# Kernel tuning notes

Measured on AMD Instinct MI355X. Metric: run time of the kernel, lower is better.

The kernel has to match this reference:

```python
import jax, jax.numpy as jnp
import numpy as np

EPS = 1e-5

def _bn_relu(z, gamma, beta):
    # BatchNorm1d (training mode: biased batch stats) + ReLU, per-feature over batch dim
    mean = jnp.mean(z, axis=0)
    var = jnp.var(z, axis=0)  # biased, matches torch BN normalization
    zn = (z - mean) * jax.lax.rsqrt(var + EPS) * gamma + beta
    return jax.nn.relu(zn)


def setup_inputs() -> dict:
    key = jax.random.key(0)
    ks = jax.random.split(key, 16)
    N, D_IN, H, D_OUT = 2097152, 16, 32, 1
    def lin(kw, kb, fan_in, fan_out):
        bound = 1.0 / np.sqrt(fan_in)
        W = jax.random.uniform(kw, (fan_out, fan_in), jnp.float32, -bound, bound)
        b = jax.random.uniform(kb, (fan_out,), jnp.float32, -bound, bound)
        return W, b
    W1, b1 = lin(ks[0], ks[1], D_IN, H)
    W2, b2 = lin(ks[2], ks[3], H, H)
    W3, b3 = lin(ks[4], ks[5], H, H)
    W4, b4 = lin(ks[6], ks[7], H, D_OUT)
    x = jax.random.normal(ks[8], (N, D_IN), jnp.float32)
    return {
        "x": x,
        "W1": W1, "b1": b1, "g1": jnp.ones((H,), jnp.float32), "be1": jnp.zeros((H,), jnp.float32),
        "W2": W2, "b2": b2, "g2": jnp.ones((H,), jnp.float32), "be2": jnp.zeros((H,), jnp.float32),
        "W3": W3, "b3": b3, "g3": jnp.ones((H,), jnp.float32), "be3": jnp.zeros((H,), jnp.float32),
        "W4": W4, "b4": b4,
    }


def reference(x, W1, b1, g1, be1, W2, b2, g2, be2, W3, b3, g3, be3, W4, b4):
    p1 = _bn_relu(x @ W1.T + b1, g1, be1)    # [N, H]
    p2 = _bn_relu(p1 @ W2.T + b2, g2, be2)   # [N, H]
    p3 = _bn_relu(p2 @ W3.T + b3, g3, be3)   # [N, H]
    return p3 @ W4.T + b4                    # [N, 1]
```

## Files before the change

### kernel.cpp

```cpp
#include <hip/hip_runtime.h>

#define EPS 1e-5f
#define NTHR 256
#define NBLK 2048
#define NSLOT 16

typedef __bf16 bf16x8 __attribute__((ext_vector_type(8)));
typedef float f32x16 __attribute__((ext_vector_type(16)));


template<int DEPTH>
__global__ __launch_bounds__(NTHR) void k_fwd(
    const float* __restrict__ x, __bf16* __restrict__ xb,
    const float* __restrict__ W1, const float* __restrict__ b1,
    const float* __restrict__ g1, const float* __restrict__ be1,
    const float* __restrict__ W2, const float* __restrict__ b2,
    const float* __restrict__ g2, const float* __restrict__ be2,
    const float* __restrict__ W3, const float* __restrict__ b3,
    const float* __restrict__ g3, const float* __restrict__ be3,
    const float* __restrict__ W4, const float* __restrict__ b4,
    float* __restrict__ stats, float* __restrict__ out, int N)
{
    constexpr bool STATS = (DEPTH < 4);
    __shared__ float s_stat[3][64];
    __shared__ float s_a[3][32];
    __shared__ float s_e[3][32];
    __shared__ float s_w[NTHR / 64][64];

    const int tid = threadIdx.x;
    const float invN = 1.0f / (float)N;

    if (tid < 64) {
        #pragma unroll
        for (int L = 0; L < DEPTH - 1; ++L) {
            float a = 0.f;
            #pragma unroll
            for (int s = 0; s < NSLOT; ++s) a += stats[L * (NSLOT * 64) + s * 64 + tid];
            s_stat[L][tid] = a;
        }
    }
    __syncthreads();
    if (tid < 32) {
        const float* gs[3]  = {g1, g2, g3};
        const float* bes[3] = {be1, be2, be3};
        const float* bs[3]  = {b1, b2, b3};
        #pragma unroll
        for (int L = 0; L < DEPTH - 1; ++L) {
            float mu = s_stat[L][tid] * invN;
            float v  = s_stat[L][32 + tid] * invN - mu * mu;
            float a  = gs[L][tid] * rsqrtf(v + EPS);
            s_a[L][tid] = a;
            s_e[L][tid] = bs[L][tid] - mu + bes[L][tid] / a;
        }
    }
    __syncthreads();

    const int lane = tid & 63;
    const int h = lane >> 5;
    const int ml = lane & 31;

    bf16x8 w1f;
    {
        const float* p = W1 + ml * 16 + h * 8;
        #pragma unroll
        for (int j = 0; j < 8; ++j) w1f[j] = (__bf16)p[j];
    }
    bf16x8 w2f0 = {}, w2f1 = {}, w3f0 = {}, w3f1 = {};
    if (DEPTH >= 2) {
        #pragma unroll
        for (int kh = 0; kh < 2; ++kh)
            #pragma unroll
            for (int j = 0; j < 8; ++j) {
                int pk = (j & 3) + 8 * (j >> 2) + 4 * h + 16 * kh;
                float v = W2[ml * 32 + pk] * s_a[0][pk];
                if (kh == 0) w2f0[j] = (__bf16)v; else w2f1[j] = (__bf16)v;
            }
    }
    if (DEPTH >= 3) {
        #pragma unroll
        for (int kh = 0; kh < 2; ++kh)
            #pragma unroll
            for (int j = 0; j < 8; ++j) {
                int pk = (j & 3) + 8 * (j >> 2) + 4 * h + 16 * kh;
                float v = W3[ml * 32 + pk] * s_a[1][pk];
                if (kh == 0) w3f0[j] = (__bf16)v; else w3f1[j] = (__bf16)v;
            }
    }

    f32x16 c1, c2 = {}, c3 = {};
    float w4c[16];
    #pragma unroll
    for (int i = 0; i < 16; ++i) {
        int p = (i & 3) + 8 * (i >> 2) + 4 * h;
        c1[i] = (DEPTH == 1) ? b1[p] : s_e[0][p];
        if (DEPTH >= 2) c2[i] = (DEPTH == 2) ? b2[p] : s_e[1][p];
        if (DEPTH >= 3) c3[i] = (DEPTH == 3) ? b3[p] : s_e[2][p];
        if (DEPTH == 4) w4c[i] = W4[p] * s_a[2][p]; else w4c[i] = 0.f;
    }
    const float b4v = (DEPTH == 4) ? b4[0] : 0.f;

    const int ntiles = N >> 5;
    const int nwaves = NBLK * (NTHR / 64);
    const int gwave  = blockIdx.x * (NTHR / 64) + (tid >> 6);
    const int tpw    = ntiles / nwaves;
    const int rem    = ntiles - tpw * nwaves;
    const int t0     = gwave * tpw + (gwave < rem ? gwave : rem);
    const int cnt    = tpw + (gwave < rem ? 1 : 0);

    float sums[16], sqs[16];
    #pragma unroll
    for (int i = 0; i < 16; ++i) { sums[i] = 0.f; sqs[i] = 0.f; }

    auto tile = [&](int t, bf16x8 xf) {
        f32x16 a1 = __builtin_amdgcn_mfma_f32_32x32x16_bf16(w1f, xf, c1, 0, 0, 0);
        if (DEPTH == 1) {
            #pragma unroll
            for (int i = 0; i < 16; ++i) { sums[i] += a1[i]; sqs[i] = fmaf(a1[i], a1[i], sqs[i]); }
            return;
        }
        bf16x8 qa, qb;
        #pragma unroll
        for (int j = 0; j < 8; ++j) {
            qa[j] = (__bf16)fmaxf(a1[j], 0.f);
            qb[j] = (__bf16)fmaxf(a1[8 + j], 0.f);
        }
        f32x16 a2 = __builtin_amdgcn_mfma_f32_32x32x16_bf16(w2f0, qa, c2, 0, 0, 0);
        a2 = __builtin_amdgcn_mfma_f32_32x32x16_bf16(w2f1, qb, a2, 0, 0, 0);
        if (DEPTH == 2) {
            #pragma unroll
            for (int i = 0; i < 16; ++i) { sums[i] += a2[i]; sqs[i] = fmaf(a2[i], a2[i], sqs[i]); }
            return;
        }
        bf16x8 pa, pb;
        #pragma unroll
        for (int j = 0; j < 8; ++j) {
            pa[j] = (__bf16)fmaxf(a2[j], 0.f);
            pb[j] = (__bf16)fmaxf(a2[8 + j], 0.f);
        }
        f32x16 a3 = __builtin_amdgcn_mfma_f32_32x32x16_bf16(w3f0, pa, c3, 0, 0, 0);
        a3 = __builtin_amdgcn_mfma_f32_32x32x16_bf16(w3f1, pb, a3, 0, 0, 0);
        if (DEPTH == 3) {
            #pragma unroll
            for (int i = 0; i < 16; ++i) { sums[i] += a3[i]; sqs[i] = fmaf(a3[i], a3[i], sqs[i]); }
            return;
        }
        float o = 0.f;
        #pragma unroll
        for (int i = 0; i < 16; ++i) o = fmaf(w4c[i], fmaxf(a3[i], 0.f), o);
        o += __shfl_xor(o, 32);
        if (h == 0) out[(t << 5) + ml] = o + b4v;
    };

    auto cvt = [&](float4 a, float4 b) -> bf16x8 {
        bf16x8 xf;
        xf[0] = (__bf16)a.x; xf[1] = (__bf16)a.y; xf[2] = (__bf16)a.z; xf[3] = (__bf16)a.w;
        xf[4] = (__bf16)b.x; xf[5] = (__bf16)b.y; xf[6] = (__bf16)b.z; xf[7] = (__bf16)b.w;
        return xf;
    };

    if (DEPTH == 1) {
        const int nb4 = cnt & ~3;
        float4 ua[4], ub[4];
        auto load4 = [&](int i0, float4* a, float4* b) {
            #pragma unroll
            for (int k = 0; k < 4; ++k) {
                const float4* p = (const float4*)(x + (size_t)((((t0 + i0 + k)) << 5) + ml) * 16 + h * 8);
                a[k] = p[0]; b[k] = p[1];
            }
        };
        auto comp4 = [&](int i0, const float4* a, const float4* b) {
            bf16x8 xf[4];
            #pragma unroll
            for (int k = 0; k < 4; ++k) xf[k] = cvt(a[k], b[k]);
            __bf16* w = xb + ((size_t)(t0 + i0) * 64 + lane) * 8;
            #pragma unroll
            for (int k = 0; k < 4; ++k) *(bf16x8*)(w + k * 512) = xf[k];
            #pragma unroll
            for (int k = 0; k < 4; ++k) tile(t0 + i0 + k, xf[k]);
        };
        int i0 = 0;
        if (nb4) load4(0, ua, ub);
        for (; i0 + 4 < nb4; i0 += 4) {
            float4 va[4], vb[4];
            load4(i0 + 4, va, vb);
            comp4(i0, ua, ub);
            #pragma unroll
            for (int k = 0; k < 4; ++k) { ua[k] = va[k]; ub[k] = vb[k]; }
        }
        if (nb4) { comp4(i0, ua, ub); i0 = nb4; }
        for (; i0 < cnt; ++i0) {
            const float4* p = (const float4*)(x + (size_t)(((t0 + i0) << 5) + ml) * 16 + h * 8);
            bf16x8 xf = cvt(p[0], p[1]);
            *(bf16x8*)(xb + ((size_t)(t0 + i0) * 64 + lane) * 8) = xf;
            tile(t0 + i0, xf);
        }
    } else {
        const int nb8 = cnt & ~7;
        int i0 = 0;
        for (; i0 < nb8; i0 += 8) {
            const __bf16* r = xb + ((size_t)(t0 + i0) * 64 + lane) * 8;
            bf16x8 v[8];
            #pragma unroll
            for (int k = 0; k < 8; ++k) v[k] = *(const bf16x8*)(r + (size_t)k * 512);
            #pragma unroll
            for (int k = 0; k < 8; ++k) tile(t0 + i0 + k, v[k]);
        }
        for (; i0 + 4 <= cnt; i0 += 4) {
            const __bf16* r = xb + ((size_t)(t0 + i0) * 64 + lane) * 8;
            bf16x8 v[4];
            #pragma unroll
            for (int k = 0; k < 4; ++k) v[k] = *(const bf16x8*)(r + (size_t)k * 512);
            #pragma unroll
            for (int k = 0; k < 4; ++k) tile(t0 + i0 + k, v[k]);
        }
        for (; i0 < cnt; ++i0) {
            bf16x8 xf = *(const bf16x8*)(xb + ((size_t)(t0 + i0) * 64 + lane) * 8);
            tile(t0 + i0, xf);
        }
    }

    if (STATS) {
        const int wid = tid >> 6;
        #pragma unroll
        for (int i = 0; i < 16; ++i) {
            float s = sums[i], q = sqs[i];
            #pragma unroll
            for (int d = 1; d <= 16; d <<= 1) {
                s += __shfl_xor(s, d);
                q += __shfl_xor(q, d);
            }
            if (ml == 0) {
                int p = (i & 3) + 8 * (i >> 2) + 4 * h;
                s_w[wid][p] = s;
                s_w[wid][32 + p] = q;
            }
        }
        __syncthreads();
        if (tid < 64) {
            float a = s_w[0][tid] + s_w[1][tid] + s_w[2][tid] + s_w[3][tid];
            int L = DEPTH - 1;
            atomicAdd(&stats[L * (NSLOT * 64) + (blockIdx.x & (NSLOT - 1)) * 64 + tid], a);
        }
    }
}

extern "C" void kernel_launch(void* const* d_in, const int* in_sizes, int n_in,
                              void* d_out, int out_size, void* d_ws, size_t ws_size,
                              hipStream_t stream) {
    const float* x   = (const float*)d_in[0];
    const float* W1  = (const float*)d_in[1];
    const float* b1  = (const float*)d_in[2];
    const float* g1  = (const float*)d_in[3];
    const float* be1 = (const float*)d_in[4];
    const float* W2  = (const float*)d_in[5];
    const float* b2  = (const float*)d_in[6];
    const float* g2  = (const float*)d_in[7];
    const float* be2 = (const float*)d_in[8];
    const float* W3  = (const float*)d_in[9];
    const float* b3  = (const float*)d_in[10];
    const float* g3  = (const float*)d_in[11];
    const float* be3 = (const float*)d_in[12];
    const float* W4  = (const float*)d_in[13];
    const float* b4  = (const float*)d_in[14];
    float* out = (float*)d_out;
    int N = in_sizes[0] / 16;

    __bf16* xb   = (__bf16*)d_ws;
    float* stats = (float*)((char*)d_ws + (size_t)N * 16 * 2);

    hipMemsetAsync(stats, 0, 3 * NSLOT * 64 * sizeof(float), stream);

    k_fwd<1><<<NBLK, NTHR, 0, stream>>>(x, xb, W1, b1, g1, be1, W2, b2, g2, be2, W3, b3, g3, be3, W4, b4, stats, out, N);
    k_fwd<2><<<NBLK, NTHR, 0, stream>>>(x, xb, W1, b1, g1, be1, W2, b2, g2, be2, W3, b3, g3, be3, W4, b4, stats, out, N);
    k_fwd<3><<<NBLK, NTHR, 0, stream>>>(x, xb, W1, b1, g1, be1, W2, b2, g2, be2, W3, b3, g3, be3, W4, b4, stats, out, N);
    k_fwd<4><<<NBLK, NTHR, 0, stream>>>(x, xb, W1, b1, g1, be1, W2, b2, g2, be2, W3, b3, g3, be3, W4, b4, stats, out, N);
}
```

Measured before the change: 367.0 us.

## Interleave MFMA chains across four tiles and halve grid size

Replaces the per-tile MFMA chain with a batch-of-four routine that issues each layer's MFMAs for four independent tiles back to back. This hides MFMA dependency latency between layers. The grid drops from 2048 to 1024 blocks, giving each wave more tiles. The software prefetch of x in the depth-1 pass and the 8-tile batching in the later passes are removed, which may expose load latency and raises register pressure.

```diff
diff --git a/kernel.cpp b/kernel.cpp
--- a/kernel.cpp
+++ b/kernel.cpp
@@ -2,7 +2,7 @@
 
 #define EPS 1e-5f
 #define NTHR 256
-#define NBLK 2048
+#define NBLK 1024
 #define NSLOT 16
 
 typedef __bf16 bf16x8 __attribute__((ext_vector_type(8)));
@@ -111,46 +111,6 @@
     #pragma unroll
     for (int i = 0; i < 16; ++i) { sums[i] = 0.f; sqs[i] = 0.f; }
 
-    auto tile = [&](int t, bf16x8 xf) {
-        f32x16 a1 = __builtin_amdgcn_mfma_f32_32x32x16_bf16(w1f, xf, c1, 0, 0, 0);
-        if (DEPTH == 1) {
-            #pragma unroll
-            for (int i = 0; i < 16; ++i) { sums[i] += a1[i]; sqs[i] = fmaf(a1[i], a1[i], sqs[i]); }
-            return;
-        }
-        bf16x8 qa, qb;
-        #pragma unroll
-        for (int j = 0; j < 8; ++j) {
-            qa[j] = (__bf16)fmaxf(a1[j], 0.f);
-            qb[j] = (__bf16)fmaxf(a1[8 + j], 0.f);
-        }
-        f32x16 a2 = __builtin_amdgcn_mfma_f32_32x32x16_bf16(w2f0, qa, c2, 0, 0, 0);
-        a2 = __builtin_amdgcn_mfma_f32_32x32x16_bf16(w2f1, qb, a2, 0, 0, 0);
-        if (DEPTH == 2) {
-            #pragma unroll
-            for (int i = 0; i < 16; ++i) { sums[i] += a2[i]; sqs[i] = fmaf(a2[i], a2[i], sqs[i]); }
-            return;
-        }
-        bf16x8 pa, pb;
-        #pragma unroll
-        for (int j = 0; j < 8; ++j) {
-            pa[j] = (__bf16)fmaxf(a2[j], 0.f);
-            pb[j] = (__bf16)fmaxf(a2[8 + j], 0.f);
-        }
-        f32x16 a3 = __builtin_amdgcn_mfma_f32_32x32x16_bf16(w3f0, pa, c3, 0, 0, 0);
-        a3 = __builtin_amdgcn_mfma_f32_32x32x16_bf16(w3f1, pb, a3, 0, 0, 0);
-        if (DEPTH == 3) {
-            #pragma unroll
-            for (int i = 0; i < 16; ++i) { sums[i] += a3[i]; sqs[i] = fmaf(a3[i], a3[i], sqs[i]); }
-            return;
-        }
-        float o = 0.f;
-        #pragma unroll
-        for (int i = 0; i < 16; ++i) o = fmaf(w4c[i], fmaxf(a3[i], 0.f), o);
-        o += __shfl_xor(o, 32);
-        if (h == 0) out[(t << 5) + ml] = o + b4v;
-    };
-
     auto cvt = [&](float4 a, float4 b) -> bf16x8 {
         bf16x8 xf;
         xf[0] = (__bf16)a.x; xf[1] = (__bf16)a.y; xf[2] = (__bf16)a.z; xf[3] = (__bf16)a.w;
@@ -158,64 +118,144 @@
         return xf;
     };
 
+    auto batch4 = [&](int tb, const bf16x8* xf) {
+        f32x16 A[4];
+        #pragma unroll
+        for (int k = 0; k < 4; ++k)
+            A[k] = __builtin_amdgcn_mfma_f32_32x32x16_bf16(w1f, xf[k], c1, 0, 0, 0);
+        if (DEPTH == 1) {
+            #pragma unroll
+            for (int k = 0; k < 4; ++k)
+                #pragma unroll
+                for (int q = 0; q < 16; ++q) { sums[q] += A[k][q]; sqs[q] = fmaf(A[k][q], A[k][q], sqs[q]); }
+            return;
+        }
+        bf16x8 qa[4], qb[4];
+        #pragma unroll
+        for (int k = 0; k < 4; ++k)
+            #pragma unroll
+            for (int j = 0; j < 8; ++j) {
+                qa[k][j] = (__bf16)fmaxf(A[k][j], 0.f);
+                qb[k][j] = (__bf16)fmaxf(A[k][8 + j], 0.f);
+            }
+        #pragma unroll
+        for (int k = 0; k < 4; ++k)
+            A[k] = __builtin_amdgcn_mfma_f32_32x32x16_bf16(w2f0, qa[k], c2, 0, 0, 0);
+        #pragma unroll
+        for (int k = 0; k < 4; ++k)
+            A[k] = __builtin_amdgcn_mfma_f32_32x32x16_bf16(w2f1, qb[k], A[k], 0, 0, 0);
+        if (DEPTH == 2) {
+            #pragma unroll
+            for (int k = 0; k < 4; ++k)
+                #pragma unroll
+                for (int q = 0; q < 16; ++q) { sums[q] += A[k][q]; sqs[q] = fmaf(A[k][q], A[k][q], sqs[q]); }
+            return;
+        }
+        #pragma unroll
+        for (int k = 0; k < 4; ++k)
+            #pragma unroll
+            for (int j = 0; j < 8; ++j) {
+                qa[k][j] = (__bf16)fmaxf(A[k][j], 0.f);
+                qb[k][j] = (__bf16)fmaxf(A[k][8 + j], 0.f);
+            }
+        #pragma unroll
+        for (int k = 0; k < 4; ++k)
+            A[k] = __builtin_amdgcn_mfma_f32_32x32x16_bf16(w3f0, qa[k], c3, 0, 0, 0);
+        #pragma unroll
+        for (int k = 0; k < 4; ++k)
+            A[k] = __builtin_amdgcn_mfma_f32_32x32x16_bf16(w3f1, qb[k], A[k], 0, 0, 0);
+        if (DEPTH == 3) {
+            #pragma unroll
+            for (int k = 0; k < 4; ++k)
+                #pragma unroll
+                for (int q = 0; q < 16; ++q) { sums[q] += A[k][q]; sqs[q] = fmaf(A[k][q], A[k][q], sqs[q]); }
+            return;
+        }
+        #pragma unroll
+        for (int k = 0; k < 4; ++k) {
+            float o = 0.f;
+            #pragma unroll
+            for (int q = 0; q < 16; ++q) o = fmaf(w4c[q], fmaxf(A[k][q], 0.f), o);
+            o += __shfl_xor(o, 32);
+            if (h == 0) out[((tb + k) << 5) + ml] = o + b4v;
+        }
+    };
+
+    auto tile1 = [&](int t, bf16x8 xf) {
+        bf16x8 xa[4] = {xf, xf, xf, xf};
+        f32x16 a1 = __builtin_amdgcn_mfma_f32_32x32x16_bf16(w1f, xf, c1, 0, 0, 0);
+        if (DEPTH == 1) {
+            #pragma unroll
+            for (int q = 0; q < 16; ++q) { sums[q] += a1[q]; sqs[q] = fmaf(a1[q], a1[q], sqs[q]); }
+            return;
+        }
+        bf16x8 qa, qb;
+        #pragma unroll
+        for (int j = 0; j < 8; ++j) {
+            qa[j] = (__bf16)fmaxf(a1[j], 0.f);
+            qb[j] = (__bf16)fmaxf(a1[8 + j], 0.f);
+        }
+        f32x16 a2 = __builtin_amdgcn_mfma_f32_32x32x16_bf16(w2f0, qa, c2, 0, 0, 0);
+        a2 = __builtin_amdgcn_mfma_f32_32x32x16_bf16(w2f1, qb, a2, 0, 0, 0);
+        if (DEPTH == 2) {
+            #pragma unroll
+            for (int q = 0; q < 16; ++q) { sums[q] += a2[q]; sqs[q] = fmaf(a2[q], a2[q], sqs[q]); }
+            return;
+        }
+        #pragma unroll
+        for (int j = 0; j < 8; ++j) {
+            qa[j] = (__bf16)fmaxf(a2[j], 0.f);
+            qb[j] = (__bf16)fmaxf(a2[8 + j], 0.f);
+        }
+        f32x16 a3 = __builtin_amdgcn_mfma_f32_32x32x16_bf16(w3f0, qa, c3, 0, 0, 0);
+        a3 = __builtin_amdgcn_mfma_f32_32x32x16_bf16(w3f1, qb, a3, 0, 0, 0);
+        if (DEPTH == 3) {
+            #pragma unroll
+            for (int q = 0; q < 16; ++q) { sums[q] += a3[q]; sqs[q] = fmaf(a3[q], a3[q], sqs[q]); }
+            return;
+        }
+        float o = 0.f;
+        #pragma unroll
+        for (int q = 0; q < 16; ++q) o = fmaf(w4c[q], fmaxf(a3[q], 0.f), o);
+        o += __shfl_xor(o, 32);
+        if (h == 0) out[(t << 5) + ml] = o + b4v;
+        (void)xa;
+    };
+
+    const int nb4 = cnt & ~3;
     if (DEPTH == 1) {
-        const int nb4 = cnt & ~3;
-        float4 ua[4], ub[4];
-        auto load4 = [&](int i0, float4* a, float4* b) {
+        for (int i0 = 0; i0 < nb4; i0 += 4) {
+            float4 u0[4], u1[4];
             #pragma unroll
             for (int k = 0; k < 4; ++k) {
-                const float4* p = (const float4*)(x + (size_t)((((t0 + i0 + k)) << 5) + ml) * 16 + h * 8);
-                a[k] = p[0]; b[k] = p[1];
-            }
-        };
-        auto comp4 = [&](int i0, const float4* a, const float4* b) {
+                const float4* p = (const float4*)(x + (size_t)(((t0 + i0 + k) << 5) + ml) * 16 + h * 8);
+                u0[k] = p[0]; u1[k] = p[1];
+            }
             bf16x8 xf[4];
             #pragma unroll
-            for (int k = 0; k < 4; ++k) xf[k] = cvt(a[k], b[k]);
+            for (int k = 0; k < 4; ++k) xf[k] = cvt(u0[k], u1[k]);
             __bf16* w = xb + ((size_t)(t0 + i0) * 64 + lane) * 8;
             #pragma unroll
             for (int k = 0; k < 4; ++k) *(bf16x8*)(w + k * 512) = xf[k];
-            #pragma unroll
-            for (int k = 0; k < 4; ++k) tile(t0 + i0 + k, xf[k]);
-        };
-        int i0 = 0;
-        if (nb4) load4(0, ua, ub);
-        for (; i0 + 4 < nb4; i0 += 4) {
-            float4 va[4], vb[4];
-            load4(i0 + 4, va, vb);
-            comp4(i0, ua, ub);
-            #pragma unroll
-            for (int k = 0; k < 4; ++k) { ua[k] = va[k]; ub[k] = vb[k]; }
-        }
-        if (nb4) { comp4(i0, ua, ub); i0 = nb4; }
-        for (; i0 < cnt; ++i0) {
-            const float4* p = (const float4*)(x + (size_t)(((t0 + i0) << 5) + ml) * 16 + h * 8);
+            batch4(t0 + i0, xf);
+        }
+        for (int i = nb4; i < cnt; ++i) {
+            const float4* p = (const float4*)(x + (size_t)(((t0 + i) << 5) + ml) * 16 + h * 8);
             bf16x8 xf = cvt(p[0], p[1]);
-            *(bf16x8*)(xb + ((size_t)(t0 + i0) * 64 + lane) * 8) = xf;
-            tile(t0 + i0, xf);
+            *(bf16x8*)(xb + ((size_t)(t0 + i) * 64 + lane) * 8) = xf;
+            tile1(t0 + i, xf);
         }
     } else {
-        const int nb8 = cnt & ~7;
-        int i0 = 0;
-        for (; i0 < nb8; i0 += 8) {
+        for (int i0 = 0; i0 < nb4; i0 += 4) {
             const __bf16* r = xb + ((size_t)(t0 + i0) * 64 + lane) * 8;
-            bf16x8 v[8];
-            #pragma unroll
-            for (int k = 0; k < 8; ++k) v[k] = *(const bf16x8*)(r + (size_t)k * 512);
-            #pragma unroll
-            for (int k = 0; k < 8; ++k) tile(t0 + i0 + k, v[k]);
-        }
-        for (; i0 + 4 <= cnt; i0 += 4) {
-            const __bf16* r = xb + ((size_t)(t0 + i0) * 64 + lane) * 8;
-            bf16x8 v[4];
-            #pragma unroll
-            for (int k = 0; k < 4; ++k) v[k] = *(const bf16x8*)(r + (size_t)k * 512);
-            #pragma unroll
-            for (int k = 0; k < 4; ++k) tile(t0 + i0 + k, v[k]);
-        }
-        for (; i0 < cnt; ++i0) {
-            bf16x8 xf = *(const bf16x8*)(xb + ((size_t)(t0 + i0) * 64 + lane) * 8);
-            tile(t0 + i0, xf);
+            bf16x8 xf[4];
+            #pragma unroll
+            for (int k = 0; k < 4; ++k) xf[k] = *(const bf16x8*)(r + (size_t)k * 512);
+            batch4(t0 + i0, xf);
+        }
+        for (int i = nb4; i < cnt; ++i) {
+            bf16x8 xf = *(const bf16x8*)(xb + ((size_t)(t0 + i) * 64 + lane) * 8);
+            tile1(t0 + i, xf);
         }
     }
 
```

Result: faster. 326.8 us (-11.0%).
